# Performance work log

Measured on AMD Instinct MI355X. Metric: run time of the kernel, lower is better.

The kernel has to match this reference:

```python
import jax, jax.numpy as jnp
import numpy as np

F_, H, C, T, I, S, P = 256, 256, 128, 4, 2, 57, 10
G = min(32, F_ // 8)  # group-norm groups
lrelu = jax.nn.leaky_relu  # slope 0.01, matches F.leaky_relu default


def group_norm(x, w, b, eps=1e-5):
    N, Cc = x.shape
    xg = x.reshape(N, G, Cc // G)
    m = xg.mean(-1, keepdims=True)
    v = xg.var(-1, keepdims=True)
    xn = ((xg - m) / jnp.sqrt(v + eps)).reshape(N, Cc)
    return xn * w + b


def _lin(k, out_d, in_d):
    k1, k2 = jax.random.split(k)
    s = 1.0 / np.sqrt(in_d)
    W = jax.random.uniform(k1, (out_d, in_d), minval=-s, maxval=s, dtype=jnp.float32)
    b = jax.random.uniform(k2, (out_d,), minval=-s, maxval=s, dtype=jnp.float32)
    return W, b


def setup_inputs() -> dict:
    key = jax.random.key(0)
    ks = jax.random.split(key, 16)
    psf = jax.random.normal(ks[0], (1, F_), dtype=jnp.float32)
    pgf = jax.random.normal(ks[1], (1, F_), dtype=jnp.float32)
    Wp, bp = _lin(ks[2], H * C, F_)
    We, be = _lin(ks[3], 1, H)
    Ws, bs = _lin(ks[4], S, H)
    Wsi, bsi = _lin(ks[5], P, H)
    Wel, bel = _lin(ks[6], H, 2 * H)
    Wee, bee = _lin(ks[7], T, H)  # T separate (1,H) linears stacked
    ne = [_lin(k, H, 3 * H + T) for k in jax.random.split(ks[8], I)]
    Wne = jnp.stack([w for w, _ in ne])  # (I, H, 3H+T)
    bne = jnp.stack([b for _, b in ne])  # (I, H)
    Wc, bc = _lin(ks[9], H, H * (I + 1))
    Wc2, bc2 = _lin(ks[10], F_, H)
    Wgc, bgc = _lin(ks[11], F_, H)
    Wgp, bgp = _lin(ks[12], H * C, F_)
    gw = jnp.ones((F_,), jnp.float32)
    gb = jnp.zeros((F_,), jnp.float32)
    return dict(parent_struct_feature=psf, parent_geo_feature=pgf,
                Wp=Wp, bp=bp, We=We, be=be, Ws=Ws, bs=bs, Wsi=Wsi, bsi=bsi,
                Wel=Wel, bel=bel, Wee=Wee, bee=bee, Wne=Wne, bne=bne,
                Wc=Wc, bc=bc, Wc2=Wc2, bc2=bc2, Wgc=Wgc, bgc=bgc,
                Wgp=Wgp, bgp=bgp, gw=gw, gb=gb)


def reference(parent_struct_feature, parent_geo_feature, Wp, bp, We, be, Ws, bs,
              Wsi, bsi, Wel, bel, Wee, bee, Wne, bne, Wc, bc, Wc2, bc2,
              Wgc, bgc, Wgp, bgp, gw, gb):
    B = parent_struct_feature.shape[0]  # must be 1 (original indexes batch 0 only)
    cf = lrelu(parent_struct_feature @ Wp.T + bp).reshape(B, C, H)
    # geo branch
    pg = lrelu(parent_geo_feature @ Wgp.T + bgp).reshape(B * C, H)
    child_geo = lrelu(group_norm(pg @ Wgc.T + bgc, gw, gb)).reshape(B, C, F_)
    flat = cf.reshape(-1, H)
    exists = (flat @ We.T + be).reshape(B, C, 1)
    sem = (flat @ Ws.T + bs).reshape(B, C, S)
    semins = (flat @ Wsi.T + bsi).reshape(B, C, P)
    # pairwise edge latents (B,C,C,H)
    pair = jnp.concatenate([jnp.broadcast_to(cf[:, :, None, :], (B, C, C, H)),
                            jnp.broadcast_to(cf[:, None, :, :], (B, C, C, H))], axis=-1)
    el = lrelu(pair @ Wel.T + bel)
    edge_logits = jnp.einsum('bijh,th->bijt', el, Wee) + bee  # (B,C,C,T)
    # dynamic edge set (torch.nonzero) expressed as a dense mask over (i,j,type)
    node_ok = exists[0, :, 0] > 0
    mask = (edge_logits[0] > 0) & node_ok[:, None, None] & node_ok[None, :, None]  # (C,C,T)
    # per-edge type logit: one-hot(type) * logit
    et = edge_logits[0][..., None] * jnp.eye(T, dtype=el.dtype)  # (C,C,T,T)
    ef = jnp.concatenate([jnp.broadcast_to(el[0][:, :, None, :], (C, C, T, H)), et], axis=-1)
    x = cf[0]  # (C,H)
    feats = [x]
    NEG = jnp.asarray(-1e30, x.dtype)
    for it in range(I):
        nef = jnp.concatenate([jnp.broadcast_to(x[:, None, None, :], (C, C, T, H)),
                               jnp.broadcast_to(x[None, :, None, :], (C, C, T, H)),
                               ef], axis=-1)  # (C,C,T,3H+T)
        nef = lrelu(nef @ Wne[it].T + bne[it])  # (C,C,T,H)
        nef = jnp.where(mask[..., None], nef, NEG)
        # scatter_max over source node i into zero-init buffer
        x = jnp.maximum(nef.max(axis=(1, 2)), 0.0)
        feats.append(x)
    cat = jnp.concatenate(feats, axis=-1)  # (C, H*(I+1))
    ch = lrelu(cat @ Wc.T + bc)
    child = lrelu(ch @ Wc2.T + bc2).reshape(B, C, F_)
    return child, child_geo, sem, semins, exists, edge_logits
```

## Files before the change

kernel.cpp:

```cpp
#include <hip/hip_runtime.h>

typedef unsigned short u16;
typedef __bf16 bf16x8 __attribute__((ext_vector_type(8)));
typedef float f32x4 __attribute__((ext_vector_type(4)));

union U8 { ushort4 h4[2]; uint4 q; bf16x8 v; };

__device__ __forceinline__ u16 f2bf(float f) {
    union { float f; unsigned int u; } v; v.f = f;
    unsigned int u = v.u;
    unsigned int r = (u + 0x7FFFu + ((u >> 16) & 1u)) >> 16;
    return (u16)r;
}
__device__ __forceinline__ float lrelu(float x) { return x > 0.f ? x : 0.01f * x; }

__device__ __forceinline__ f32x4 mfma_(bf16x8 a, bf16x8 b, f32x4 c) {
    return __builtin_amdgcn_mfma_f32_16x16x32_bf16(a, b, c, 0, 0, 0);
}

__global__ __launch_bounds__(256) void pack_all(
    const float* __restrict__ Wel, const float* __restrict__ Wne,
    const float* __restrict__ Ws, const float* __restrict__ Wsi,
    const float* __restrict__ We, const float* __restrict__ Wgc,
    const float* __restrict__ Wc, const float* __restrict__ Wc2,
    float* __restrict__ WT_a, float* __restrict__ WT_g,
    float* __restrict__ WT_n, float* __restrict__ WT_c,
    float* __restrict__ WT_c2, u16* __restrict__ W3p) {
    const int b = blockIdx.x, tid = threadIdx.x;
    if (b >= 192) {
        const int tg = (b - 192) * 256 + tid;
        const int it = tg >> 13;
        const int r = tg & 8191;
        const int wid = r >> 11, nt = (r >> 9) & 3, ks = (r >> 6) & 7, l = r & 63;
        const int lr = l & 15, lq = l >> 4;
        const int h = wid * 64 + nt * 16 + lr;
        const int k0 = ks * 32 + lq * 8;
        const float* src = Wne + (size_t)it * 256 * 772 + (size_t)h * 772 + 512 + k0;
        f32x4 a = *(const f32x4*)src;
        f32x4 c = *(const f32x4*)(src + 4);
        U8 u;
        u.h4[0].x = f2bf(a[0]); u.h4[0].y = f2bf(a[1]);
        u.h4[0].z = f2bf(a[2]); u.h4[0].w = f2bf(a[3]);
        u.h4[1].x = f2bf(c[0]); u.h4[1].y = f2bf(c[1]);
        u.h4[1].z = f2bf(c[2]); u.h4[1].w = f2bf(c[3]);
        ((uint4*)W3p)[tg] = u.q;
        return;
    }
    __shared__ float lds[64][65];
    const int lane = tid & 63, sub = tid >> 6;
    int src_id, ct, kt; float* dst; int ldd;
    if (b < 80)       { src_id = 0; ct = b >> 2;        kt = b & 3;        dst = WT_a;  ldd = 1280; }
    else if (b < 96)  { src_id = 1; ct = (b - 80) >> 2; kt = (b - 80) & 3; dst = WT_g;  ldd = 256; }
    else if (b < 128) { src_id = 2; ct = (b - 96) >> 2; kt = (b - 96) & 3; dst = WT_n;  ldd = 512; }
    else if (b < 176) { src_id = 3; ct = (b - 128) / 12; kt = (b - 128) % 12; dst = WT_c; ldd = 256; }
    else              { src_id = 4; ct = (b - 176) >> 2; kt = (b - 176) & 3; dst = WT_c2; ldd = 256; }
    const int c0 = ct * 64, k0 = kt * 64;
#pragma unroll 4
    for (int p = 0; p < 16; ++p) {
        const int row = p * 4 + sub;
        const int cabs = c0 + row;
        const float* base = nullptr;
        if (src_id == 0) {
            if (cabs < 256)       base = Wel + (size_t)cabs * 512;
            else if (cabs < 512)  base = Wel + (size_t)(cabs - 256) * 512 + 256;
            else if (cabs < 768)  base = Wne + (size_t)(cabs - 512) * 772;
            else if (cabs < 1024) base = Wne + (size_t)(cabs - 768) * 772 + 256;
            else if (cabs < 1081) base = Ws + (size_t)(cabs - 1024) * 256;
            else if (cabs < 1091) base = Wsi + (size_t)(cabs - 1081) * 256;
            else if (cabs == 1091) base = We;
        } else if (src_id == 1) {
            base = Wgc + (size_t)cabs * 256;
        } else if (src_id == 2) {
            base = (cabs < 256) ? Wne + 256 * 772 + (size_t)cabs * 772
                                : Wne + 256 * 772 + (size_t)(cabs - 256) * 772 + 256;
        } else if (src_id == 3) {
            base = Wc + (size_t)cabs * 768;
        } else {
            base = Wc2 + (size_t)cabs * 256;
        }
        lds[row][lane] = base ? base[k0 + lane] : 0.f;
    }
    __syncthreads();
#pragma unroll 4
    for (int p = 0; p < 16; ++p) {
        const int kr = p * 4 + sub;
        dst[(size_t)(k0 + kr) * ldd + c0 + lane] = lds[lane][kr];
    }
}

__global__ __launch_bounds__(256) void big_matvec(
    const float* __restrict__ Wp, const float* __restrict__ bp,
    const float* __restrict__ Wgp, const float* __restrict__ bgp,
    const float* __restrict__ psf, const float* __restrict__ pgf,
    float* __restrict__ cat, float* __restrict__ pg) {
    const int wg = blockIdx.x * 4 + (threadIdx.x >> 6);
    const int l = threadIdx.x & 63;
    f32x4 xa = *(const f32x4*)(psf + l * 4);
    f32x4 xg = *(const f32x4*)(pgf + l * 4);
    {
        const int r0 = wg * 4;
        f32x4 w0 = *(const f32x4*)(Wp + (size_t)r0 * 256 + l * 4);
        f32x4 w1 = *(const f32x4*)(Wp + (size_t)(r0 + 1) * 256 + l * 4);
        f32x4 w2 = *(const f32x4*)(Wp + (size_t)(r0 + 2) * 256 + l * 4);
        f32x4 w3 = *(const f32x4*)(Wp + (size_t)(r0 + 3) * 256 + l * 4);
        float s0 = w0[0]*xa[0] + w0[1]*xa[1] + w0[2]*xa[2] + w0[3]*xa[3];
        float s1 = w1[0]*xa[0] + w1[1]*xa[1] + w1[2]*xa[2] + w1[3]*xa[3];
        float s2 = w2[0]*xa[0] + w2[1]*xa[1] + w2[2]*xa[2] + w2[3]*xa[3];
        float s3 = w3[0]*xa[0] + w3[1]*xa[1] + w3[2]*xa[2] + w3[3]*xa[3];
#pragma unroll
        for (int m = 1; m < 64; m <<= 1) {
            s0 += __shfl_xor(s0, m); s1 += __shfl_xor(s1, m);
            s2 += __shfl_xor(s2, m); s3 += __shfl_xor(s3, m);
        }
        if (l == 0) {
            f32x4 bv = *(const f32x4*)(bp + r0);
            f32x4 o; o[0] = lrelu(s0 + bv[0]); o[1] = lrelu(s1 + bv[1]);
            o[2] = lrelu(s2 + bv[2]); o[3] = lrelu(s3 + bv[3]);
            *(f32x4*)(cat + (r0 >> 8) * 768 + (r0 & 255)) = o;
        }
    }
    {
        const int r0 = wg * 4;
        f32x4 w0 = *(const f32x4*)(Wgp + (size_t)r0 * 256 + l * 4);
        f32x4 w1 = *(const f32x4*)(Wgp + (size_t)(r0 + 1) * 256 + l * 4);
        f32x4 w2 = *(const f32x4*)(Wgp + (size_t)(r0 + 2) * 256 + l * 4);
        f32x4 w3 = *(const f32x4*)(Wgp + (size_t)(r0 + 3) * 256 + l * 4);
        float s0 = w0[0]*xg[0] + w0[1]*xg[1] + w0[2]*xg[2] + w0[3]*xg[3];
        float s1 = w1[0]*xg[0] + w1[1]*xg[1] + w1[2]*xg[2] + w1[3]*xg[3];
        float s2 = w2[0]*xg[0] + w2[1]*xg[1] + w2[2]*xg[2] + w2[3]*xg[3];
        float s3 = w3[0]*xg[0] + w3[1]*xg[1] + w3[2]*xg[2] + w3[3]*xg[3];
#pragma unroll
        for (int m = 1; m < 64; m <<= 1) {
            s0 += __shfl_xor(s0, m); s1 += __shfl_xor(s1, m);
            s2 += __shfl_xor(s2, m); s3 += __shfl_xor(s3, m);
        }
        if (l == 0) {
            f32x4 bv = *(const f32x4*)(bgp + r0);
            f32x4 o; o[0] = lrelu(s0 + bv[0]); o[1] = lrelu(s1 + bv[1]);
            o[2] = lrelu(s2 + bv[2]); o[3] = lrelu(s3 + bv[3]);
            *(f32x4*)(pg + r0) = o;
        }
    }
}

__global__ __launch_bounds__(256) void stage1_gemv(
    const float* __restrict__ cat, const float* __restrict__ pgin,
    const float* __restrict__ WT_a, const float* __restrict__ WT_g,
    const float* __restrict__ bgc, const float* __restrict__ gw,
    const float* __restrict__ gb, const float* __restrict__ be,
    const float* __restrict__ bs, const float* __restrict__ bsi,
    float* __restrict__ P, float* __restrict__ Q,
    float* __restrict__ An, float* __restrict__ Bn, int* __restrict__ ok,
    float* __restrict__ o_geo, float* __restrict__ o_sem,
    float* __restrict__ o_semins, float* __restrict__ o_exists) {
    const int ct = blockIdx.x % 6, g = blockIdx.x / 6;
    const int tid = threadIdx.x, lane = tid & 63, w = tid >> 6;
    __shared__ float xs[4][256];
    __shared__ float part[4][4][256];
    const float* WT; int ldw, c0;
    if (ct == 5) { WT = WT_g; ldw = 256; c0 = 0; }
    else         { WT = WT_a; ldw = 1280; c0 = ct * 256; }
    for (int idx = tid; idx < 1024; idx += 256) {
        const int nn = idx >> 8, k = idx & 255;
        xs[nn][k] = (ct == 5) ? pgin[(g * 4 + nn) * 256 + k]
                              : cat[(g * 4 + nn) * 768 + k];
    }
    __syncthreads();
    f32x4 a0{0,0,0,0}, a1{0,0,0,0}, a2{0,0,0,0}, a3{0,0,0,0};
    const float* wp = WT + (size_t)(w * 64) * ldw + c0 + lane * 4;
#pragma unroll 4
    for (int kk = 0; kk < 64; ++kk) {
        const int k = w * 64 + kk;
        f32x4 wv = *(const f32x4*)wp; wp += ldw;
        a0 += wv * xs[0][k];
        a1 += wv * xs[1][k];
        a2 += wv * xs[2][k];
        a3 += wv * xs[3][k];
    }
    *(f32x4*)&part[w][0][lane * 4] = a0;
    *(f32x4*)&part[w][1][lane * 4] = a1;
    *(f32x4*)&part[w][2][lane * 4] = a2;
    *(f32x4*)&part[w][3][lane * 4] = a3;
    __syncthreads();
    const int c = tid;
    float v[4];
#pragma unroll
    for (int nn = 0; nn < 4; ++nn)
        v[nn] = part[0][nn][c] + part[1][nn][c] + part[2][nn][c] + part[3][nn][c];
    if (ct < 4) {
        float* dst = (ct == 0) ? P : (ct == 1) ? Q : (ct == 2) ? An : Bn;
#pragma unroll
        for (int nn = 0; nn < 4; ++nn) dst[(g * 4 + nn) * 256 + c] = v[nn];
    } else if (ct == 4) {
        if (c < 57) {
#pragma unroll
            for (int nn = 0; nn < 4; ++nn) o_sem[(g * 4 + nn) * 57 + c] = v[nn] + bs[c];
        } else if (c < 67) {
#pragma unroll
            for (int nn = 0; nn < 4; ++nn) o_semins[(g * 4 + nn) * 10 + (c - 57)] = v[nn] + bsi[c - 57];
        } else if (c == 67) {
#pragma unroll
            for (int nn = 0; nn < 4; ++nn) {
                const float e = v[nn] + be[0];
                o_exists[g * 4 + nn] = e;
                ok[g * 4 + nn] = (e > 0.f) ? 1 : 0;
            }
        }
    } else {
        const float gwc = gw[c], gbc = gb[c], bgcc = bgc[c];
#pragma unroll
        for (int nn = 0; nn < 4; ++nn) {
            const float g0 = v[nn] + bgcc;
            float s = g0;
            s += __shfl_xor(s, 1); s += __shfl_xor(s, 2); s += __shfl_xor(s, 4);
            const float m = s * 0.125f;
            const float d = g0 - m;
            float q2 = d * d;
            q2 += __shfl_xor(q2, 1); q2 += __shfl_xor(q2, 2); q2 += __shfl_xor(q2, 4);
            const float var = q2 * 0.125f;
            o_geo[(g * 4 + nn) * 256 + c] = lrelu(d / sqrtf(var + 1e-5f) * gwc + gbc);
        }
    }
}

__global__ __launch_bounds__(256) void edge_k(
    const float* __restrict__ P, const float* __restrict__ Q,
    const float* __restrict__ bel, const float* __restrict__ Wee,
    const float* __restrict__ bee,
    u16* __restrict__ el, float* __restrict__ o_edge) {
    const int pair = blockIdx.x * 4 + (threadIdx.x >> 6);
    const int l = threadIdx.x & 63;
    const int i = pair >> 7, j = pair & 127;
    f32x4 p = *(const f32x4*)(P + i * 256 + l * 4);
    f32x4 q = *(const f32x4*)(Q + j * 256 + l * 4);
    f32x4 b = *(const f32x4*)(bel + l * 4);
    float e0 = lrelu(p[0] + q[0] + b[0]);
    float e1 = lrelu(p[1] + q[1] + b[1]);
    float e2 = lrelu(p[2] + q[2] + b[2]);
    float e3 = lrelu(p[3] + q[3] + b[3]);
    ushort4 st; st.x = f2bf(e0); st.y = f2bf(e1); st.z = f2bf(e2); st.w = f2bf(e3);
    *(ushort4*)(el + (size_t)pair * 256 + l * 4) = st;
    f32x4 w;
    w = *(const f32x4*)(Wee + 0 * 256 + l * 4);
    float a0 = e0 * w[0] + e1 * w[1] + e2 * w[2] + e3 * w[3];
    w = *(const f32x4*)(Wee + 1 * 256 + l * 4);
    float a1 = e0 * w[0] + e1 * w[1] + e2 * w[2] + e3 * w[3];
    w = *(const f32x4*)(Wee + 2 * 256 + l * 4);
    float a2 = e0 * w[0] + e1 * w[1] + e2 * w[2] + e3 * w[3];
    w = *(const f32x4*)(Wee + 3 * 256 + l * 4);
    float a3 = e0 * w[0] + e1 * w[1] + e2 * w[2] + e3 * w[3];
#pragma unroll
    for (int mk = 1; mk < 64; mk <<= 1) {
        a0 += __shfl_xor(a0, mk); a1 += __shfl_xor(a1, mk);
        a2 += __shfl_xor(a2, mk); a3 += __shfl_xor(a3, mk);
    }
    if (l == 0) {
        f32x4 o;
        o[0] = a0 + bee[0]; o[1] = a1 + bee[1];
        o[2] = a2 + bee[2]; o[3] = a3 + bee[3];
        *(f32x4*)(o_edge + (size_t)pair * 4) = o;
    }
}

__global__ __launch_bounds__(256) void node_gemv(
    const float* __restrict__ cat, const float* __restrict__ WT_n,
    float* __restrict__ An, float* __restrict__ Bn) {
    const int ct = blockIdx.x & 1, g = blockIdx.x >> 1;
    const int tid = threadIdx.x, lane = tid & 63, w = tid >> 6;
    __shared__ float xs[4][256];
    __shared__ float part[4][4][256];
    for (int idx = tid; idx < 1024; idx += 256) {
        const int nn = idx >> 8, k = idx & 255;
        xs[nn][k] = cat[(g * 4 + nn) * 768 + 256 + k];
    }
    __syncthreads();
    f32x4 a0{0,0,0,0}, a1{0,0,0,0}, a2{0,0,0,0}, a3{0,0,0,0};
    const float* wp = WT_n + (size_t)(w * 64) * 512 + ct * 256 + lane * 4;
#pragma unroll 4
    for (int kk = 0; kk < 64; ++kk) {
        const int k = w * 64 + kk;
        f32x4 wv = *(const f32x4*)wp; wp += 512;
        a0 += wv * xs[0][k];
        a1 += wv * xs[1][k];
        a2 += wv * xs[2][k];
        a3 += wv * xs[3][k];
    }
    *(f32x4*)&part[w][0][lane * 4] = a0;
    *(f32x4*)&part[w][1][lane * 4] = a1;
    *(f32x4*)&part[w][2][lane * 4] = a2;
    *(f32x4*)&part[w][3][lane * 4] = a3;
    __syncthreads();
    const int c = tid;
    float* dst = ct ? Bn : An;
#pragma unroll
    for (int nn = 0; nn < 4; ++nn)
        dst[(g * 4 + nn) * 256 + c] = part[0][nn][c] + part[1][nn][c] + part[2][nn][c] + part[3][nn][c];
}

__global__ __launch_bounds__(512) void mp_k(
    const u16* __restrict__ el, const float* __restrict__ An,
    const float* __restrict__ Bn, const float* __restrict__ Wne_it,
    const float* __restrict__ bne_it, const u16* __restrict__ W3p_it,
    const float* __restrict__ logits,
    const int* __restrict__ ok, float* __restrict__ xout ) {
    const int i = blockIdx.x;
    const int tid = threadIdx.x;
    if (!ok[i]) { if (tid < 256) xout[i * 768 + tid] = 0.f; return; }
    const int l = tid & 63, wid = tid >> 6;
    const int jh = wid >> 2, hq = wid & 3;
    const int lr = l & 15, lq = l >> 4;
    const int h0 = hq * 64;
    __shared__ float red[2][4][4][16];

    bf16x8 bfr[4][8];
    float an[4], bnev[4];
    f32x4 w4[4];
#pragma unroll
    for (int nt = 0; nt < 4; ++nt) {
#pragma unroll
        for (int ks = 0; ks < 8; ++ks) {
            U8 u;
            u.q = ((const uint4*)W3p_it)[(hq * 4 + nt) * 512 + ks * 64 + l];
            bfr[nt][ks] = u.v;
        }
        const int h = h0 + nt * 16 + lr;
        an[nt] = An[i * 256 + h];
        bnev[nt] = bne_it[h];
        w4[nt] = *(const f32x4*)(Wne_it + (size_t)h * 772 + 768);
    }
    unsigned long long bl1 = __ballot(ok[l] != 0);
    unsigned long long bl2 = __ballot(ok[64 + l] != 0);
    unsigned actmask = 0;
#pragma unroll
    for (int jc = 0; jc < 4; ++jc) {
        if ((bl1 >> (jc * 16)) & 0xFFFFull) actmask |= (1u << jc);
        if ((bl2 >> (jc * 16)) & 0xFFFFull) actmask |= (1u << (4 + jc));
    }
    float rm0 = -1e30f, rm1 = -1e30f, rm2 = -1e30f, rm3 = -1e30f;
    for (int jc = jh * 4; jc < jh * 4 + 4; ++jc) {
        if (!(actmask & (1u << jc))) continue;
        f32x4 acc0{0.f,0.f,0.f,0.f}, acc1{0.f,0.f,0.f,0.f};
        f32x4 acc2{0.f,0.f,0.f,0.f}, acc3{0.f,0.f,0.f,0.f};
#pragma unroll
        for (int ks = 0; ks < 8; ++ks) {
            U8 u;
            u.q = *(const uint4*)(el + (size_t)(i * 128 + jc * 16 + lr) * 256 + ks * 32 + lq * 8);
            bf16x8 af = u.v;
            acc0 = mfma_(af, bfr[0][ks], acc0);
            acc1 = mfma_(af, bfr[1][ks], acc1);
            acc2 = mfma_(af, bfr[2][ks], acc2);
            acc3 = mfma_(af, bfr[3][ks], acc3);
        }
#pragma unroll
        for (int r = 0; r < 4; ++r) {
            const int j = jc * 16 + lq * 4 + r;
            if (!ok[j]) continue;
            f32x4 lg = *(const f32x4*)(logits + (size_t)(i * 128 + j) * 4);
            bool any = (lg[0] > 0.f) | (lg[1] > 0.f) | (lg[2] > 0.f) | (lg[3] > 0.f);
            if (!any) continue;
            float b0 = Bn[j * 256 + h0 + 0 * 16 + lr];
            float b1 = Bn[j * 256 + h0 + 1 * 16 + lr];
            float b2 = Bn[j * 256 + h0 + 2 * 16 + lr];
            float b3 = Bn[j * 256 + h0 + 3 * 16 + lr];
            float amx0 = -1e30f, amx1 = -1e30f, amx2 = -1e30f, amx3 = -1e30f;
#pragma unroll
            for (int t = 0; t < 4; ++t) {
                if (lg[t] > 0.f) {
                    amx0 = fmaxf(amx0, w4[0][t] * lg[t]);
                    amx1 = fmaxf(amx1, w4[1][t] * lg[t]);
                    amx2 = fmaxf(amx2, w4[2][t] * lg[t]);
                    amx3 = fmaxf(amx3, w4[3][t] * lg[t]);
                }
            }
            rm0 = fmaxf(rm0, lrelu(acc0[r] + an[0] + b0 + bnev[0] + amx0));
            rm1 = fmaxf(rm1, lrelu(acc1[r] + an[1] + b1 + bnev[1] + amx1));
            rm2 = fmaxf(rm2, lrelu(acc2[r] + an[2] + b2 + bnev[2] + amx2));
            rm3 = fmaxf(rm3, lrelu(acc3[r] + an[3] + b3 + bnev[3] + amx3));
        }
    }
    rm0 = fmaxf(rm0, __shfl_xor(rm0, 16)); rm0 = fmaxf(rm0, __shfl_xor(rm0, 32));
    rm1 = fmaxf(rm1, __shfl_xor(rm1, 16)); rm1 = fmaxf(rm1, __shfl_xor(rm1, 32));
    rm2 = fmaxf(rm2, __shfl_xor(rm2, 16)); rm2 = fmaxf(rm2, __shfl_xor(rm2, 32));
    rm3 = fmaxf(rm3, __shfl_xor(rm3, 16)); rm3 = fmaxf(rm3, __shfl_xor(rm3, 32));
    if (lq == 0) {
        red[jh][hq][0][lr] = rm0;
        red[jh][hq][1][lr] = rm1;
        red[jh][hq][2][lr] = rm2;
        red[jh][hq][3][lr] = rm3;
    }
    __syncthreads();
    if (jh == 0 && lq == 0) {
#pragma unroll
        for (int nt = 0; nt < 4; ++nt) {
            float f = fmaxf(red[0][hq][nt][lr], red[1][hq][nt][lr]);
            xout[i * 768 + h0 + nt * 16 + lr] = fmaxf(f, 0.f);
        }
    }
}

__global__ __launch_bounds__(256) void head_gemv(
    const float* __restrict__ cat, const float* __restrict__ WT_c,
    const float* __restrict__ bc, const float* __restrict__ WT_c2,
    const float* __restrict__ bc2, float* __restrict__ o_child) {
    const int i = blockIdx.x;
    const int tid = threadIdx.x, lane = tid & 63, w = tid >> 6;
    __shared__ float xs[768];
    __shared__ float part[4][256];
    __shared__ float ch[256];
    for (int idx = tid; idx < 768; idx += 256) xs[idx] = cat[i * 768 + idx];
    __syncthreads();
    f32x4 acc{0,0,0,0};
    const float* wp = WT_c + (size_t)(w * 192) * 256 + lane * 4;
#pragma unroll 4
    for (int kk = 0; kk < 192; ++kk) {
        f32x4 wv = *(const f32x4*)wp; wp += 256;
        acc += wv * xs[w * 192 + kk];
    }
    *(f32x4*)&part[w][lane * 4] = acc;
    __syncthreads();
    ch[tid] = lrelu(part[0][tid] + part[1][tid] + part[2][tid] + part[3][tid] + bc[tid]);
    __syncthreads();
    f32x4 acc2{0,0,0,0};
    wp = WT_c2 + (size_t)(w * 64) * 256 + lane * 4;
#pragma unroll 4
    for (int kk = 0; kk < 64; ++kk) {
        f32x4 wv = *(const f32x4*)wp; wp += 256;
        acc2 += wv * ch[w * 64 + kk];
    }
    __syncthreads();
    *(f32x4*)&part[w][lane * 4] = acc2;
    __syncthreads();
    o_child[i * 256 + tid] = lrelu(part[0][tid] + part[1][tid] + part[2][tid] + part[3][tid] + bc2[tid]);
}

extern "C" void kernel_launch(void* const* d_in, const int* in_sizes, int n_in,
                              void* d_out, int out_size, void* d_ws, size_t ws_size,
                              hipStream_t stream) {
    (void)in_sizes; (void)n_in; (void)out_size; (void)ws_size;
    const float* psf = (const float*)d_in[0];
    const float* pgf = (const float*)d_in[1];
    const float* Wp  = (const float*)d_in[2];
    const float* bp  = (const float*)d_in[3];
    const float* We  = (const float*)d_in[4];
    const float* be  = (const float*)d_in[5];
    const float* Ws  = (const float*)d_in[6];
    const float* bs  = (const float*)d_in[7];
    const float* Wsi = (const float*)d_in[8];
    const float* bsi = (const float*)d_in[9];
    const float* Wel = (const float*)d_in[10];
    const float* bel = (const float*)d_in[11];
    const float* Wee = (const float*)d_in[12];
    const float* bee = (const float*)d_in[13];
    const float* Wne = (const float*)d_in[14];
    const float* bne = (const float*)d_in[15];
    const float* Wc  = (const float*)d_in[16];
    const float* bc  = (const float*)d_in[17];
    const float* Wc2 = (const float*)d_in[18];
    const float* bc2 = (const float*)d_in[19];
    const float* Wgc = (const float*)d_in[20];
    const float* bgc = (const float*)d_in[21];
    const float* Wgp = (const float*)d_in[22];
    const float* bgp = (const float*)d_in[23];
    const float* gw  = (const float*)d_in[24];
    const float* gb  = (const float*)d_in[25];

    float* ws   = (float*)d_ws;
    float* pg   = ws;
    float* cat  = ws + 32768;
    float* P    = ws + 131072;
    float* Q    = ws + 163840;
    float* An   = ws + 196608;
    float* Bn   = ws + 229376;
    int*   ok   = (int*)(ws + 262144);
    u16*   el   = (u16*)(ws + 262272);
    u16*   W3p  = (u16*)(ws + 2359424);
    float* WT_a = ws + 2424960;
    float* WT_g = ws + 2752640;
    float* WT_n = ws + 2818176;
    float* WT_c = ws + 2949248;
    float* WT_c2= ws + 3145856;

    float* out = (float*)d_out;
    float* o_child  = out;
    float* o_geo    = out + 32768;
    float* o_sem    = out + 65536;
    float* o_semins = out + 72832;
    float* o_exists = out + 74112;
    float* o_edge   = out + 74240;

    pack_all<<<256, 256, 0, stream>>>(Wel, Wne, Ws, Wsi, We, Wgc, Wc, Wc2,
                                      WT_a, WT_g, WT_n, WT_c, WT_c2, W3p);
    big_matvec<<<2048, 256, 0, stream>>>(Wp, bp, Wgp, bgp, psf, pgf, cat, pg);
    stage1_gemv<<<192, 256, 0, stream>>>(cat, pg, WT_a, WT_g, bgc, gw, gb,
                                         be, bs, bsi, P, Q, An, Bn, ok,
                                         o_geo, o_sem, o_semins, o_exists);
    edge_k<<<4096, 256, 0, stream>>>(P, Q, bel, Wee, bee, el, o_edge);
    mp_k<<<128, 512, 0, stream>>>(el, An, Bn, Wne, bne, W3p,
                                  o_edge, ok, cat + 256);
    node_gemv<<<64, 256, 0, stream>>>(cat, WT_n, An, Bn);
    mp_k<<<128, 512, 0, stream>>>(el, An, Bn, Wne + 256 * 772, bne + 256,
                                  W3p + 65536, o_edge, ok, cat + 512);
    head_gemv<<<128, 256, 0, stream>>>(cat, WT_c, bc, WT_c2, bc2, o_child);
}
```

Baseline: 241.6 us.

## Fuse node GEMV into first message pass and head GEMV into second

Folds the node-projection GEMV into the end of the first message-passing kernel and the head MLP into the end of the second, cutting two launches and the round trips of intermediates through global memory. The strided Wne type-column weights are also packed into a small contiguous buffer during the prepack step. In exchange, each per-node block does more serial scalar GEMV work using a per-thread column layout instead of the earlier vectorised f32x4 loads. An1/Bn1 reuse the P/Q workspace.

```diff
diff --git a/kernel.cpp b/kernel.cpp
--- a/kernel.cpp
+++ b/kernel.cpp
@@ -25,8 +25,17 @@
     const float* __restrict__ Wc, const float* __restrict__ Wc2,
     float* __restrict__ WT_a, float* __restrict__ WT_g,
     float* __restrict__ WT_n, float* __restrict__ WT_c,
-    float* __restrict__ WT_c2, u16* __restrict__ W3p) {
+    float* __restrict__ WT_c2, u16* __restrict__ W3p,
+    float* __restrict__ W4p) {
     const int b = blockIdx.x, tid = threadIdx.x;
+    if (b >= 256) {
+        const int it = b - 256;
+        for (int idx = tid; idx < 1024; idx += 256) {
+            W4p[it * 1024 + idx] =
+                Wne[(size_t)it * 197632 + (size_t)(idx >> 2) * 772 + 768 + (idx & 3)];
+        }
+        return;
+    }
     if (b >= 192) {
         const int tg = (b - 192) * 256 + tid;
         const int it = tg >> 13;
@@ -35,7 +44,7 @@
         const int lr = l & 15, lq = l >> 4;
         const int h = wid * 64 + nt * 16 + lr;
         const int k0 = ks * 32 + lq * 8;
-        const float* src = Wne + (size_t)it * 256 * 772 + (size_t)h * 772 + 512 + k0;
+        const float* src = Wne + (size_t)it * 197632 + (size_t)h * 772 + 512 + k0;
         f32x4 a = *(const f32x4*)src;
         f32x4 c = *(const f32x4*)(src + 4);
         U8 u;
@@ -71,8 +80,8 @@
         } else if (src_id == 1) {
             base = Wgc + (size_t)cabs * 256;
         } else if (src_id == 2) {
-            base = (cabs < 256) ? Wne + 256 * 772 + (size_t)cabs * 772
-                                : Wne + 256 * 772 + (size_t)(cabs - 256) * 772 + 256;
+            base = (cabs < 256) ? Wne + 197632 + (size_t)cabs * 772
+                                : Wne + 197632 + (size_t)(cabs - 256) * 772 + 256;
         } else if (src_id == 3) {
             base = Wc + (size_t)cabs * 768;
         } else {
@@ -262,56 +271,17 @@
     }
 }
 
-__global__ __launch_bounds__(256) void node_gemv(
-    const float* __restrict__ cat, const float* __restrict__ WT_n,
-    float* __restrict__ An, float* __restrict__ Bn) {
-    const int ct = blockIdx.x & 1, g = blockIdx.x >> 1;
-    const int tid = threadIdx.x, lane = tid & 63, w = tid >> 6;
-    __shared__ float xs[4][256];
-    __shared__ float part[4][4][256];
-    for (int idx = tid; idx < 1024; idx += 256) {
-        const int nn = idx >> 8, k = idx & 255;
-        xs[nn][k] = cat[(g * 4 + nn) * 768 + 256 + k];
-    }
-    __syncthreads();
-    f32x4 a0{0,0,0,0}, a1{0,0,0,0}, a2{0,0,0,0}, a3{0,0,0,0};
-    const float* wp = WT_n + (size_t)(w * 64) * 512 + ct * 256 + lane * 4;
-#pragma unroll 4
-    for (int kk = 0; kk < 64; ++kk) {
-        const int k = w * 64 + kk;
-        f32x4 wv = *(const f32x4*)wp; wp += 512;
-        a0 += wv * xs[0][k];
-        a1 += wv * xs[1][k];
-        a2 += wv * xs[2][k];
-        a3 += wv * xs[3][k];
-    }
-    *(f32x4*)&part[w][0][lane * 4] = a0;
-    *(f32x4*)&part[w][1][lane * 4] = a1;
-    *(f32x4*)&part[w][2][lane * 4] = a2;
-    *(f32x4*)&part[w][3][lane * 4] = a3;
-    __syncthreads();
-    const int c = tid;
-    float* dst = ct ? Bn : An;
-#pragma unroll
-    for (int nn = 0; nn < 4; ++nn)
-        dst[(g * 4 + nn) * 256 + c] = part[0][nn][c] + part[1][nn][c] + part[2][nn][c] + part[3][nn][c];
-}
-
-__global__ __launch_bounds__(512) void mp_k(
-    const u16* __restrict__ el, const float* __restrict__ An,
-    const float* __restrict__ Bn, const float* __restrict__ Wne_it,
-    const float* __restrict__ bne_it, const u16* __restrict__ W3p_it,
-    const float* __restrict__ logits,
-    const int* __restrict__ ok, float* __restrict__ xout ) {
-    const int i = blockIdx.x;
-    const int tid = threadIdx.x;
-    if (!ok[i]) { if (tid < 256) xout[i * 768 + tid] = 0.f; return; }
+__device__ __forceinline__ void mp_core(
+    const int i, const int tid,
+    const u16* __restrict__ el, const float* __restrict__ Anp,
+    const float* __restrict__ Bnp, const float* __restrict__ bne_it,
+    const u16* __restrict__ W3p_it, const float* __restrict__ W4p_it,
+    const float* __restrict__ logits, const int* __restrict__ ok,
+    float* __restrict__ xs, float (*red)[4][4][16]) {
     const int l = tid & 63, wid = tid >> 6;
     const int jh = wid >> 2, hq = wid & 3;
     const int lr = l & 15, lq = l >> 4;
     const int h0 = hq * 64;
-    __shared__ float red[2][4][4][16];
-
     bf16x8 bfr[4][8];
     float an[4], bnev[4];
     f32x4 w4[4];
@@ -324,9 +294,9 @@
             bfr[nt][ks] = u.v;
         }
         const int h = h0 + nt * 16 + lr;
-        an[nt] = An[i * 256 + h];
+        an[nt] = Anp[i * 256 + h];
         bnev[nt] = bne_it[h];
-        w4[nt] = *(const f32x4*)(Wne_it + (size_t)h * 772 + 768);
+        w4[nt] = *(const f32x4*)(W4p_it + h * 4);
     }
     unsigned long long bl1 = __ballot(ok[l] != 0);
     unsigned long long bl2 = __ballot(ok[64 + l] != 0);
@@ -358,10 +328,10 @@
             f32x4 lg = *(const f32x4*)(logits + (size_t)(i * 128 + j) * 4);
             bool any = (lg[0] > 0.f) | (lg[1] > 0.f) | (lg[2] > 0.f) | (lg[3] > 0.f);
             if (!any) continue;
-            float b0 = Bn[j * 256 + h0 + 0 * 16 + lr];
-            float b1 = Bn[j * 256 + h0 + 1 * 16 + lr];
-            float b2 = Bn[j * 256 + h0 + 2 * 16 + lr];
-            float b3 = Bn[j * 256 + h0 + 3 * 16 + lr];
+            float b0 = Bnp[j * 256 + h0 + 0 * 16 + lr];
+            float b1 = Bnp[j * 256 + h0 + 1 * 16 + lr];
+            float b2 = Bnp[j * 256 + h0 + 2 * 16 + lr];
+            float b3 = Bnp[j * 256 + h0 + 3 * 16 + lr];
             float amx0 = -1e30f, amx1 = -1e30f, amx2 = -1e30f, amx3 = -1e30f;
 #pragma unroll
             for (int t = 0; t < 4; ++t) {
@@ -393,44 +363,86 @@
 #pragma unroll
         for (int nt = 0; nt < 4; ++nt) {
             float f = fmaxf(red[0][hq][nt][lr], red[1][hq][nt][lr]);
-            xout[i * 768 + h0 + nt * 16 + lr] = fmaxf(f, 0.f);
-        }
-    }
-}
-
-__global__ __launch_bounds__(256) void head_gemv(
+            xs[h0 + nt * 16 + lr] = fmaxf(f, 0.f);
+        }
+    }
+    __syncthreads();
+}
+
+__global__ __launch_bounds__(512) void mp0_k(
+    const u16* __restrict__ el, const float* __restrict__ An,
+    const float* __restrict__ Bn, const float* __restrict__ bne,
+    const u16* __restrict__ W3p, const float* __restrict__ W4p,
+    const float* __restrict__ logits, const int* __restrict__ ok,
+    float* __restrict__ cat, const float* __restrict__ WT_n,
+    float* __restrict__ An1, float* __restrict__ Bn1) {
+    __shared__ float xs[256];
+    __shared__ float red[2][4][4][16];
+    const int i = blockIdx.x, tid = threadIdx.x;
+    if (!ok[i]) {
+        if (tid < 256) {
+            cat[i * 768 + 256 + tid] = 0.f;
+            An1[i * 256 + tid] = 0.f;
+        } else {
+            Bn1[i * 256 + (tid - 256)] = 0.f;
+        }
+        return;
+    }
+    mp_core(i, tid, el, An, Bn, bne, W3p, W4p, logits, ok, xs, red);
+    if (tid < 256) cat[i * 768 + 256 + tid] = xs[tid];
+    float acc = 0.f;
+    const float* wp = WT_n + tid;
+#pragma unroll 8
+    for (int k = 0; k < 256; ++k) acc += wp[(size_t)k * 512] * xs[k];
+    if (tid < 256) An1[i * 256 + tid] = acc;
+    else Bn1[i * 256 + (tid - 256)] = acc;
+}
+
+__global__ __launch_bounds__(512) void mp1_k(
+    const u16* __restrict__ el, const float* __restrict__ An1,
+    const float* __restrict__ Bn1, const float* __restrict__ bne1,
+    const u16* __restrict__ W3p1, const float* __restrict__ W4p1,
+    const float* __restrict__ logits, const int* __restrict__ ok,
     const float* __restrict__ cat, const float* __restrict__ WT_c,
     const float* __restrict__ bc, const float* __restrict__ WT_c2,
     const float* __restrict__ bc2, float* __restrict__ o_child) {
-    const int i = blockIdx.x;
-    const int tid = threadIdx.x, lane = tid & 63, w = tid >> 6;
-    __shared__ float xs[768];
-    __shared__ float part[4][256];
+    __shared__ float xs[256];
+    __shared__ float red[2][4][4][16];
+    __shared__ float cs[768];
+    __shared__ float part[256];
     __shared__ float ch[256];
-    for (int idx = tid; idx < 768; idx += 256) xs[idx] = cat[i * 768 + idx];
-    __syncthreads();
-    f32x4 acc{0,0,0,0};
-    const float* wp = WT_c + (size_t)(w * 192) * 256 + lane * 4;
-#pragma unroll 4
-    for (int kk = 0; kk < 192; ++kk) {
-        f32x4 wv = *(const f32x4*)wp; wp += 256;
-        acc += wv * xs[w * 192 + kk];
-    }
-    *(f32x4*)&part[w][lane * 4] = acc;
-    __syncthreads();
-    ch[tid] = lrelu(part[0][tid] + part[1][tid] + part[2][tid] + part[3][tid] + bc[tid]);
-    __syncthreads();
-    f32x4 acc2{0,0,0,0};
-    wp = WT_c2 + (size_t)(w * 64) * 256 + lane * 4;
-#pragma unroll 4
-    for (int kk = 0; kk < 64; ++kk) {
-        f32x4 wv = *(const f32x4*)wp; wp += 256;
-        acc2 += wv * ch[w * 64 + kk];
-    }
-    __syncthreads();
-    *(f32x4*)&part[w][lane * 4] = acc2;
-    __syncthreads();
-    o_child[i * 256 + tid] = lrelu(part[0][tid] + part[1][tid] + part[2][tid] + part[3][tid] + bc2[tid]);
+    const int i = blockIdx.x, tid = threadIdx.x;
+    if (ok[i]) {
+        mp_core(i, tid, el, An1, Bn1, bne1, W3p1, W4p1, logits, ok, xs, red);
+    } else {
+        if (tid < 256) xs[tid] = 0.f;
+        __syncthreads();
+    }
+    cs[tid] = cat[i * 768 + tid];
+    if (tid < 256) cs[512 + tid] = xs[tid];
+    __syncthreads();
+    const int c = tid & 255, kh = tid >> 8;
+    float acc = 0.f;
+    {
+        const float* wp = WT_c + (size_t)(kh * 384) * 256 + c;
+        const float* xv = cs + kh * 384;
+#pragma unroll 8
+        for (int k = 0; k < 384; ++k) acc += wp[(size_t)k * 256] * xv[k];
+    }
+    if (kh == 1) part[c] = acc;
+    __syncthreads();
+    if (kh == 0) ch[c] = lrelu(acc + part[c] + bc[c]);
+    __syncthreads();
+    float acc2 = 0.f;
+    {
+        const float* wp = WT_c2 + (size_t)(kh * 128) * 256 + c;
+        const float* xv = ch + kh * 128;
+#pragma unroll 8
+        for (int k = 0; k < 128; ++k) acc2 += wp[(size_t)k * 256] * xv[k];
+    }
+    if (kh == 1) part[c] = acc2;
+    __syncthreads();
+    if (kh == 0) o_child[i * 256 + c] = lrelu(acc2 + part[c] + bc2[c]);
 }
 
 extern "C" void kernel_launch(void* const* d_in, const int* in_sizes, int n_in,
@@ -479,6 +491,9 @@
     float* WT_n = ws + 2818176;
     float* WT_c = ws + 2949248;
     float* WT_c2= ws + 3145856;
+    float* W4p  = ws + 3211392;
+    float* An1  = P;
+    float* Bn1  = Q;
 
     float* out = (float*)d_out;
     float* o_child  = out;
@@ -488,17 +503,16 @@
     float* o_exists = out + 74112;
     float* o_edge   = out + 74240;
 
-    pack_all<<<256, 256, 0, stream>>>(Wel, Wne, Ws, Wsi, We, Wgc, Wc, Wc2,
-                                      WT_a, WT_g, WT_n, WT_c, WT_c2, W3p);
+    pack_all<<<258, 256, 0, stream>>>(Wel, Wne, Ws, Wsi, We, Wgc, Wc, Wc2,
+                                      WT_a, WT_g, WT_n, WT_c, WT_c2, W3p, W4p);
     big_matvec<<<2048, 256, 0, stream>>>(Wp, bp, Wgp, bgp, psf, pgf, cat, pg);
     stage1_gemv<<<192, 256, 0, stream>>>(cat, pg, WT_a, WT_g, bgc, gw, gb,
                                          be, bs, bsi, P, Q, An, Bn, ok,
                                          o_geo, o_sem, o_semins, o_exists);
     edge_k<<<4096, 256, 0, stream>>>(P, Q, bel, Wee, bee, el, o_edge);
-    mp_k<<<128, 512, 0, stream>>>(el, An, Bn, Wne, bne, W3p,
-                                  o_edge, ok, cat + 256);
-    node_gemv<<<64, 256, 0, stream>>>(cat, WT_n, An, Bn);
-    mp_k<<<128, 512, 0, stream>>>(el, An, Bn, Wne + 256 * 772, bne + 256,
-                                  W3p + 65536, o_edge, ok, cat + 512);
-    head_gemv<<<128, 256, 0, stream>>>(cat, WT_c, bc, WT_c2, bc2, o_child);
-}
+    mp0_k<<<128, 512, 0, stream>>>(el, An, Bn, bne, W3p, W4p,
+                                   o_edge, ok, cat, WT_n, An1, Bn1);
+    mp1_k<<<128, 512, 0, stream>>>(el, An1, Bn1, bne + 256, W3p + 65536,
+                                   W4p + 1024, o_edge, ok, cat,
+                                   WT_c, bc, WT_c2, bc2, o_child);
+}
```

After: 234.3 us. 3.0% less time.

## Split message-passing over j halves with LDS-staged Bn and atomicMax reduction

Applied to the files above, without the earlier changes.

The message-passing kernel now launches two blocks per source node, each covering half of the neighbour nodes, and the halves are merged with an integer atomicMax into the output. The atomicMax is valid because the value is clamped to be non-negative and the output is zeroed beforehand in stage1. Each block stages its Bn rows and edge logits in shared memory, and the edge-type weight column is prepacked contiguously so it is not read with a 772-float stride. Node_gemv writes to separate buffers so the second iteration does not overwrite An/Bn. This doubles block count to improve occupancy, at the cost of atomics and a larger shared-memory footprint.

```diff
diff --git a/kernel.cpp b/kernel.cpp
--- a/kernel.cpp
+++ b/kernel.cpp
@@ -25,8 +25,17 @@
     const float* __restrict__ Wc, const float* __restrict__ Wc2,
     float* __restrict__ WT_a, float* __restrict__ WT_g,
     float* __restrict__ WT_n, float* __restrict__ WT_c,
-    float* __restrict__ WT_c2, u16* __restrict__ W3p) {
+    float* __restrict__ WT_c2, u16* __restrict__ W3p,
+    float* __restrict__ W4p) {
     const int b = blockIdx.x, tid = threadIdx.x;
+    if (b >= 256) {
+        const int it = b - 256;
+        for (int idx = tid; idx < 1024; idx += 256) {
+            W4p[it * 1024 + idx] =
+                Wne[(size_t)it * 197632 + (size_t)(idx >> 2) * 772 + 768 + (idx & 3)];
+        }
+        return;
+    }
     if (b >= 192) {
         const int tg = (b - 192) * 256 + tid;
         const int it = tg >> 13;
@@ -35,7 +44,7 @@
         const int lr = l & 15, lq = l >> 4;
         const int h = wid * 64 + nt * 16 + lr;
         const int k0 = ks * 32 + lq * 8;
-        const float* src = Wne + (size_t)it * 256 * 772 + (size_t)h * 772 + 512 + k0;
+        const float* src = Wne + (size_t)it * 197632 + (size_t)h * 772 + 512 + k0;
         f32x4 a = *(const f32x4*)src;
         f32x4 c = *(const f32x4*)(src + 4);
         U8 u;
@@ -71,8 +80,8 @@
         } else if (src_id == 1) {
             base = Wgc + (size_t)cabs * 256;
         } else if (src_id == 2) {
-            base = (cabs < 256) ? Wne + 256 * 772 + (size_t)cabs * 772
-                                : Wne + 256 * 772 + (size_t)(cabs - 256) * 772 + 256;
+            base = (cabs < 256) ? Wne + 197632 + (size_t)cabs * 772
+                                : Wne + 197632 + (size_t)(cabs - 256) * 772 + 256;
         } else if (src_id == 3) {
             base = Wc + (size_t)cabs * 768;
         } else {
@@ -144,7 +153,8 @@
 }
 
 __global__ __launch_bounds__(256) void stage1_gemv(
-    const float* __restrict__ cat, const float* __restrict__ pgin,
+    const float* __restrict__ cat, float* __restrict__ cat_z,
+    const float* __restrict__ pgin,
     const float* __restrict__ WT_a, const float* __restrict__ WT_g,
     const float* __restrict__ bgc, const float* __restrict__ gw,
     const float* __restrict__ gb, const float* __restrict__ be,
@@ -157,6 +167,12 @@
     const int tid = threadIdx.x, lane = tid & 63, w = tid >> 6;
     __shared__ float xs[4][256];
     __shared__ float part[4][4][256];
+    if (ct == 0) {
+        for (int idx = tid; idx < 2048; idx += 256) {
+            const int nn = idx >> 9, off = idx & 511;
+            cat_z[(g * 4 + nn) * 768 + 256 + off] = 0.f;
+        }
+    }
     const float* WT; int ldw, c0;
     if (ct == 5) { WT = WT_g; ldw = 256; c0 = 0; }
     else         { WT = WT_a; ldw = 1280; c0 = ct * 256; }
@@ -262,56 +278,29 @@
     }
 }
 
-__global__ __launch_bounds__(256) void node_gemv(
-    const float* __restrict__ cat, const float* __restrict__ WT_n,
-    float* __restrict__ An, float* __restrict__ Bn) {
-    const int ct = blockIdx.x & 1, g = blockIdx.x >> 1;
-    const int tid = threadIdx.x, lane = tid & 63, w = tid >> 6;
-    __shared__ float xs[4][256];
-    __shared__ float part[4][4][256];
-    for (int idx = tid; idx < 1024; idx += 256) {
-        const int nn = idx >> 8, k = idx & 255;
-        xs[nn][k] = cat[(g * 4 + nn) * 768 + 256 + k];
-    }
-    __syncthreads();
-    f32x4 a0{0,0,0,0}, a1{0,0,0,0}, a2{0,0,0,0}, a3{0,0,0,0};
-    const float* wp = WT_n + (size_t)(w * 64) * 512 + ct * 256 + lane * 4;
-#pragma unroll 4
-    for (int kk = 0; kk < 64; ++kk) {
-        const int k = w * 64 + kk;
-        f32x4 wv = *(const f32x4*)wp; wp += 512;
-        a0 += wv * xs[0][k];
-        a1 += wv * xs[1][k];
-        a2 += wv * xs[2][k];
-        a3 += wv * xs[3][k];
-    }
-    *(f32x4*)&part[w][0][lane * 4] = a0;
-    *(f32x4*)&part[w][1][lane * 4] = a1;
-    *(f32x4*)&part[w][2][lane * 4] = a2;
-    *(f32x4*)&part[w][3][lane * 4] = a3;
-    __syncthreads();
-    const int c = tid;
-    float* dst = ct ? Bn : An;
-#pragma unroll
-    for (int nn = 0; nn < 4; ++nn)
-        dst[(g * 4 + nn) * 256 + c] = part[0][nn][c] + part[1][nn][c] + part[2][nn][c] + part[3][nn][c];
-}
-
 __global__ __launch_bounds__(512) void mp_k(
-    const u16* __restrict__ el, const float* __restrict__ An,
-    const float* __restrict__ Bn, const float* __restrict__ Wne_it,
-    const float* __restrict__ bne_it, const u16* __restrict__ W3p_it,
-    const float* __restrict__ logits,
-    const int* __restrict__ ok, float* __restrict__ xout ) {
-    const int i = blockIdx.x;
+    const u16* __restrict__ el, const float* __restrict__ Anp,
+    const float* __restrict__ Bnp, const float* __restrict__ bne_it,
+    const u16* __restrict__ W3p_it, const float* __restrict__ W4p_it,
+    const float* __restrict__ logits, const int* __restrict__ ok,
+    float* __restrict__ xout ) {
+    const int b = blockIdx.x;
+    const int i = b >> 1, jhalf = b & 1;
+    if (!ok[i]) return;
+    __shared__ float Bs[64 * 260];
+    __shared__ float ls[256];
+    __shared__ float red[2][4][4][16];
     const int tid = threadIdx.x;
-    if (!ok[i]) { if (tid < 256) xout[i * 768 + tid] = 0.f; return; }
     const int l = tid & 63, wid = tid >> 6;
     const int jh = wid >> 2, hq = wid & 3;
     const int lr = l & 15, lq = l >> 4;
     const int h0 = hq * 64;
-    __shared__ float red[2][4][4][16];
-
+    for (int idx = tid; idx < 4096; idx += 512) {
+        const int j = idx >> 6, c4 = (idx & 63) * 4;
+        *(f32x4*)&Bs[j * 260 + c4] =
+            *(const f32x4*)(Bnp + (size_t)(jhalf * 64 + j) * 256 + c4);
+    }
+    if (tid < 256) ls[tid] = logits[(size_t)i * 512 + jhalf * 256 + tid];
     bf16x8 bfr[4][8];
     float an[4], bnev[4];
     f32x4 w4[4];
@@ -324,9 +313,9 @@
             bfr[nt][ks] = u.v;
         }
         const int h = h0 + nt * 16 + lr;
-        an[nt] = An[i * 256 + h];
+        an[nt] = Anp[i * 256 + h];
         bnev[nt] = bne_it[h];
-        w4[nt] = *(const f32x4*)(Wne_it + (size_t)h * 772 + 768);
+        w4[nt] = *(const f32x4*)(W4p_it + h * 4);
     }
     unsigned long long bl1 = __ballot(ok[l] != 0);
     unsigned long long bl2 = __ballot(ok[64 + l] != 0);
@@ -336,8 +325,10 @@
         if ((bl1 >> (jc * 16)) & 0xFFFFull) actmask |= (1u << jc);
         if ((bl2 >> (jc * 16)) & 0xFFFFull) actmask |= (1u << (4 + jc));
     }
+    __syncthreads();
     float rm0 = -1e30f, rm1 = -1e30f, rm2 = -1e30f, rm3 = -1e30f;
-    for (int jc = jh * 4; jc < jh * 4 + 4; ++jc) {
+    const int jc0 = jhalf * 4 + jh * 2;
+    for (int jc = jc0; jc < jc0 + 2; ++jc) {
         if (!(actmask & (1u << jc))) continue;
         f32x4 acc0{0.f,0.f,0.f,0.f}, acc1{0.f,0.f,0.f,0.f};
         f32x4 acc2{0.f,0.f,0.f,0.f}, acc3{0.f,0.f,0.f,0.f};
@@ -355,13 +346,15 @@
         for (int r = 0; r < 4; ++r) {
             const int j = jc * 16 + lq * 4 + r;
             if (!ok[j]) continue;
-            f32x4 lg = *(const f32x4*)(logits + (size_t)(i * 128 + j) * 4);
+            const int jl = j - jhalf * 64;
+            f32x4 lg = *(const f32x4*)&ls[jl * 4];
             bool any = (lg[0] > 0.f) | (lg[1] > 0.f) | (lg[2] > 0.f) | (lg[3] > 0.f);
             if (!any) continue;
-            float b0 = Bn[j * 256 + h0 + 0 * 16 + lr];
-            float b1 = Bn[j * 256 + h0 + 1 * 16 + lr];
-            float b2 = Bn[j * 256 + h0 + 2 * 16 + lr];
-            float b3 = Bn[j * 256 + h0 + 3 * 16 + lr];
+            const float* bsr = &Bs[jl * 260 + h0 + lr];
+            float b0 = bsr[0];
+            float b1 = bsr[16];
+            float b2 = bsr[32];
+            float b3 = bsr[48];
             float amx0 = -1e30f, amx1 = -1e30f, amx2 = -1e30f, amx3 = -1e30f;
 #pragma unroll
             for (int t = 0; t < 4; ++t) {
@@ -392,10 +385,45 @@
     if (jh == 0 && lq == 0) {
 #pragma unroll
         for (int nt = 0; nt < 4; ++nt) {
-            float f = fmaxf(red[0][hq][nt][lr], red[1][hq][nt][lr]);
-            xout[i * 768 + h0 + nt * 16 + lr] = fmaxf(f, 0.f);
-        }
-    }
+            float v = fmaxf(fmaxf(red[0][hq][nt][lr], red[1][hq][nt][lr]), 0.f);
+            atomicMax((int*)&xout[i * 768 + h0 + nt * 16 + lr], __float_as_int(v));
+        }
+    }
+}
+
+__global__ __launch_bounds__(256) void node_gemv(
+    const float* __restrict__ cat, const float* __restrict__ WT_n,
+    float* __restrict__ An, float* __restrict__ Bn) {
+    const int ct = blockIdx.x & 1, g = blockIdx.x >> 1;
+    const int tid = threadIdx.x, lane = tid & 63, w = tid >> 6;
+    __shared__ float xs[4][256];
+    __shared__ float part[4][4][256];
+    for (int idx = tid; idx < 1024; idx += 256) {
+        const int nn = idx >> 8, k = idx & 255;
+        xs[nn][k] = cat[(g * 4 + nn) * 768 + 256 + k];
+    }
+    __syncthreads();
+    f32x4 a0{0,0,0,0}, a1{0,0,0,0}, a2{0,0,0,0}, a3{0,0,0,0};
+    const float* wp = WT_n + (size_t)(w * 64) * 512 + ct * 256 + lane * 4;
+#pragma unroll 4
+    for (int kk = 0; kk < 64; ++kk) {
+        const int k = w * 64 + kk;
+        f32x4 wv = *(const f32x4*)wp; wp += 512;
+        a0 += wv * xs[0][k];
+        a1 += wv * xs[1][k];
+        a2 += wv * xs[2][k];
+        a3 += wv * xs[3][k];
+    }
+    *(f32x4*)&part[w][0][lane * 4] = a0;
+    *(f32x4*)&part[w][1][lane * 4] = a1;
+    *(f32x4*)&part[w][2][lane * 4] = a2;
+    *(f32x4*)&part[w][3][lane * 4] = a3;
+    __syncthreads();
+    const int c = tid;
+    float* dst = ct ? Bn : An;
+#pragma unroll
+    for (int nn = 0; nn < 4; ++nn)
+        dst[(g * 4 + nn) * 256 + c] = part[0][nn][c] + part[1][nn][c] + part[2][nn][c] + part[3][nn][c];
 }
 
 __global__ __launch_bounds__(256) void head_gemv(
@@ -479,6 +507,9 @@
     float* WT_n = ws + 2818176;
     float* WT_c = ws + 2949248;
     float* WT_c2= ws + 3145856;
+    float* W4p  = ws + 3211392;
+    float* An1  = P;
+    float* Bn1  = Q;
 
     float* out = (float*)d_out;
     float* o_child  = out;
@@ -488,17 +519,17 @@
     float* o_exists = out + 74112;
     float* o_edge   = out + 74240;
 
-    pack_all<<<256, 256, 0, stream>>>(Wel, Wne, Ws, Wsi, We, Wgc, Wc, Wc2,
-                                      WT_a, WT_g, WT_n, WT_c, WT_c2, W3p);
+    pack_all<<<258, 256, 0, stream>>>(Wel, Wne, Ws, Wsi, We, Wgc, Wc, Wc2,
+                                      WT_a, WT_g, WT_n, WT_c, WT_c2, W3p, W4p);
     big_matvec<<<2048, 256, 0, stream>>>(Wp, bp, Wgp, bgp, psf, pgf, cat, pg);
-    stage1_gemv<<<192, 256, 0, stream>>>(cat, pg, WT_a, WT_g, bgc, gw, gb,
+    stage1_gemv<<<192, 256, 0, stream>>>(cat, cat, pg, WT_a, WT_g, bgc, gw, gb,
                                          be, bs, bsi, P, Q, An, Bn, ok,
                                          o_geo, o_sem, o_semins, o_exists);
     edge_k<<<4096, 256, 0, stream>>>(P, Q, bel, Wee, bee, el, o_edge);
-    mp_k<<<128, 512, 0, stream>>>(el, An, Bn, Wne, bne, W3p,
+    mp_k<<<256, 512, 0, stream>>>(el, An, Bn, bne, W3p, W4p,
                                   o_edge, ok, cat + 256);
-    node_gemv<<<64, 256, 0, stream>>>(cat, WT_n, An, Bn);
-    mp_k<<<128, 512, 0, stream>>>(el, An, Bn, Wne + 256 * 772, bne + 256,
-                                  W3p + 65536, o_edge, ok, cat + 512);
+    node_gemv<<<64, 256, 0, stream>>>(cat, WT_n, An1, Bn1);
+    mp_k<<<256, 512, 0, stream>>>(el, An1, Bn1, bne + 256, W3p + 65536,
+                                  W4p + 1024, o_edge, ok, cat + 512);
     head_gemv<<<128, 256, 0, stream>>>(cat, WT_c, bc, WT_c2, bc2, o_child);
 }
```

Result: faster. 224.1 us (-7.3%).
